# Performance work log

Hardware: AMD Instinct MI355X
Metric: run time of the kernel (lower is better)

Reference implementation:

```python
import jax, jax.numpy as jnp
import numpy as np

BS, HIST, H, W, NOBJ = 512, 3, 10, 10, 4
NSENT, TOK, DM = 3, 36, 768
EMB, FM, K, NL, ADIM = 256, 64, 2, 128, 5
LIN = FM * (H - (K - 1)) * (W - (K - 1))  # 64*9*9 = 5184
ATTN_SCALE = float(np.sqrt(EMB))  # 16.0


def setup_inputs() -> dict:
    key = jax.random.key(0)
    ks = jax.random.split(key, 24)
    g = lambda i, shape, s=0.02: jax.random.normal(ks[i], shape, dtype=jnp.float32) * s
    sprite_emb = g(0, (25, EMB), 1.0).at[0].set(0.0)  # padding_idx=0 -> zero row
    inp = {
        'state': jax.random.randint(ks[1], (BS, HIST, H, W, NOBJ), 0, 25, dtype=jnp.int32),
        'action': jax.random.randint(ks[2], (BS,), 0, ADIM, dtype=jnp.int32),
        'temb': jax.random.normal(ks[3], (BS, NSENT, TOK, DM), dtype=jnp.float32),
        'sprite_emb': sprite_emb,
        'conv_w': g(4, (K, K, HIST * EMB, FM)),  # HWIO
        'conv_b': g(5, (FM,)),
        'Wk': g(6, (DM, EMB)), 'bk': g(7, (EMB,)),
        'Wks': g(8, (DM, 1)), 'bks': g(9, (1,)),
        'Wv': g(10, (DM, EMB)), 'bv': g(11, (EMB,)),
        'Wvs': g(12, (DM, 1)), 'bvs': g(13, (1,)),
        'a1': g(14, (LIN, NL)), 'a1b': g(15, (NL,)),
        'a2': g(16, (NL, NL)), 'a2b': g(17, (NL,)),
        'a3': g(18, (NL, ADIM)), 'a3b': g(19, (ADIM,)),
        'v1': g(20, (LIN, NL)), 'v1b': g(21, (NL,)),
        'v2': g(22, (NL, NL)), 'v2b': g(23, (NL,)),
        'v3': jax.random.normal(jax.random.fold_in(key, 99), (NL, 1)) * 0.02,
        'v3b': jnp.zeros((1,), jnp.float32),
    }
    return inp


def _nonzero_mean(e):
    # e: [..., n, emb]; mean over rows that are nonzero (padding rows are all-zero)
    cnt = jnp.sum(jnp.sum(e, axis=-1) != 0, axis=-1, keepdims=True)
    return jnp.sum(e, axis=-2) / jnp.maximum(cnt, 1).astype(e.dtype)


def reference(state, action, temb, sprite_emb, conv_w, conv_b, Wk, bk, Wks, bks,
              Wv, bv, Wvs, bvs, a1, a1b, a2, a2b, a3, a3b, v1, v1b, v2, v2b, v3, v3b):
    lrelu = jax.nn.leaky_relu  # slope 0.01 matches torch default
    bs = state.shape[0]
    obj_state, avt_state = state[..., :-1], state[..., -1:]
    query = _nonzero_mean(sprite_emb[obj_state])   # [bs,hist,H,W,emb]
    avatar = _nonzero_mean(sprite_emb[avt_state])  # [bs,hist,H,W,emb]
    # text key/value: scaled token-softmax pooling over tokens (dim=2)
    k = (temb @ Wk + bk) * jax.nn.softmax(temb @ Wks + bks, axis=-2)
    k = jnp.sum(k, axis=2)                          # [bs,nsent,emb]
    v = (temb @ Wv + bv) * jax.nn.softmax(temb @ Wvs + bvs, axis=-2)
    v = jnp.sum(v, axis=2)                          # [bs,nsent,emb]
    # batch_attention
    q2 = query.reshape(bs, -1, EMB)                 # [bs, hist*H*W, emb]
    kq = jnp.einsum('bxe,bse->bxs', q2, k) / ATTN_SCALE
    wts = jax.nn.softmax(kq, axis=-1) * (kq != 0)
    wts = wts.reshape(bs, HIST, H, W, NSENT)
    # mean(weights[...,None]*value, dim=-2) == (w @ v) / nsent
    att = jnp.einsum('bthws,bse->bthwe', wts, v) / NSENT  # [bs,hist,H,W,emb]
    st = att.reshape(bs, H, W, -1)                  # fold hist into channels (768)
    av = avatar.reshape(bs, H, W, -1)
    st = (st + av) / 2.0                            # NHWC, C=768
    y = jax.lax.conv_general_dilated(st, conv_w, (1, 1), 'VALID',
                                     dimension_numbers=('NHWC', 'HWIO', 'NHWC')) + conv_b
    y = lrelu(y)                                    # [bs,9,9,64]
    y = jnp.transpose(y, (0, 3, 1, 2)).reshape(bs, -1)  # torch NCHW flatten order
    ha = lrelu(lrelu(y @ a1 + a1b) @ a2 + a2b)
    logits = ha @ a3 + a3b
    logp = jax.nn.log_softmax(logits, axis=-1)
    action_logprobs = jnp.take_along_axis(logp, action[:, None].astype(jnp.int32), axis=-1)[:, 0]
    entropy = -jnp.sum(jnp.exp(logp) * logp, axis=-1)
    hv = lrelu(lrelu(y @ v1 + v1b) @ v2 + v2b)
    state_value = (hv @ v3 + v3b)[:, 0]
    return action_logprobs, state_value, entropy
```

## Files before the change

### kernel.cpp

```cpp
#include <hip/hip_runtime.h>
#include <hip/hip_bf16.h>
#include <math.h>

constexpr int BS   = 512;
constexpr int NBS  = 1536;
constexpr int NPOS = 300;
constexpr int LIN  = 5184;
constexpr int KSPLIT = 9, KCH = 576;

typedef __attribute__((ext_vector_type(8))) short bf16x8;
typedef __attribute__((ext_vector_type(4))) float f32x4;

static __device__ __forceinline__ short f2bf(float f) {
    unsigned u = __float_as_uint(f);
    unsigned r = (u + 0x7FFFu + ((u >> 16) & 1u)) >> 16;
    return (short)r;
}
static __device__ __forceinline__ unsigned pk2(float a, float b) {
    return ((unsigned)(unsigned short)f2bf(a)) | (((unsigned)(unsigned short)f2bf(b)) << 16);
}
static __device__ __forceinline__ float bf2f_lo(unsigned u) { return __uint_as_float(u << 16); }
static __device__ __forceinline__ float bf2f_hi(unsigned u) { return __uint_as_float(u & 0xFFFF0000u); }

constexpr size_t OFF_RD   = 0;
constexpr size_t OFF_FL   = 19968;
constexpr size_t OFF_DT   = 20032;
constexpr size_t OFF_WCT  = 118336;
constexpr size_t OFF_PH   = 413248;
constexpr size_t OFF_AB   = 437824;
constexpr size_t OFF_XKH  = 1101376;
constexpr size_t OFF_XVH  = 1691200;
constexpr size_t OFF_VWH  = 2281024;
constexpr size_t OFF_YH   = 2870848;
constexpr size_t OFF_PART = 4197952;

__global__ __launch_bounds__(512) void k1_fused(
    const float* __restrict__ temb, const float* __restrict__ Wks,
    const float* __restrict__ Wvs, const float* __restrict__ conv_w,
    const float* __restrict__ sprite, const float* __restrict__ Wk,
    const float* __restrict__ Wv, const float* __restrict__ bv,
    const float* __restrict__ a1, const float* __restrict__ v1,
    short* __restrict__ XKH, short* __restrict__ XVH,
    short* __restrict__ AB, short* __restrict__ PH, short* __restrict__ WCT,
    float* __restrict__ RD, int* __restrict__ FL)
{
    __shared__ unsigned smem[13824 + 160];
    unsigned* hbuf = smem;
    float (*sco)[40] = (float(*)[40])(smem + 13824);
    int tid = threadIdx.x, bx = blockIdx.x;
    int lane = tid & 63, w = tid >> 6;

    if (bx < NBS) {
        int bs = bx;
        const float4* src4 = (const float4*)temb + (size_t)bs * 6912;

        #pragma unroll
        for (int c = 0; c < 7; ++c) {
            int i = c * 512 + tid;
            if (c < 6 || tid < 384) {
                float4 v = src4[i];
                hbuf[2 * i]     = pk2(v.x, v.y);
                hbuf[2 * i + 1] = pk2(v.z, v.w);
            }
        }
        __syncthreads();

        float4 q0, q1, q2, q3, q4, q5, q6 = make_float4(0.f, 0.f, 0.f, 0.f);
        q0 = src4[3456 + tid];
        q1 = src4[3968 + tid];
        q2 = src4[4480 + tid];
        q3 = src4[4992 + tid];
        q4 = src4[5504 + tid];
        q5 = src4[6016 + tid];
        if (tid < 384) q6 = src4[6528 + tid];

        const float2* wks2 = (const float2*)Wks;
        const float2* wvs2 = (const float2*)Wvs;
        #pragma unroll
        for (int rr = 0; rr < 3; ++rr) {
            int t = w + 8 * rr;
            if (rr < 2 || w < 2) {
                float pk = 0.f, pv = 0.f;
                #pragma unroll
                for (int j = 0; j < 6; ++j) {
                    unsigned u = hbuf[t * 384 + lane + 64 * j];
                    float x0 = bf2f_lo(u), x1 = bf2f_hi(u);
                    float2 a = wks2[lane + 64 * j];
                    float2 b = wvs2[lane + 64 * j];
                    pk += x0 * a.x + x1 * a.y;
                    pv += x0 * b.x + x1 * b.y;
                }
                #pragma unroll
                for (int off = 32; off; off >>= 1) {
                    pk += __shfl_down(pk, off);
                    pv += __shfl_down(pv, off);
                }
                if (lane == 0) { sco[0][t] = pk; sco[1][t] = pv; }
            }
        }

        hbuf[2 * (3456 + tid)]     = pk2(q0.x, q0.y);
        hbuf[2 * (3456 + tid) + 1] = pk2(q0.z, q0.w);
        hbuf[2 * (3968 + tid)]     = pk2(q1.x, q1.y);
        hbuf[2 * (3968 + tid) + 1] = pk2(q1.z, q1.w);
        hbuf[2 * (4480 + tid)]     = pk2(q2.x, q2.y);
        hbuf[2 * (4480 + tid) + 1] = pk2(q2.z, q2.w);
        hbuf[2 * (4992 + tid)]     = pk2(q3.x, q3.y);
        hbuf[2 * (4992 + tid) + 1] = pk2(q3.z, q3.w);
        hbuf[2 * (5504 + tid)]     = pk2(q4.x, q4.y);
        hbuf[2 * (5504 + tid) + 1] = pk2(q4.z, q4.w);
        hbuf[2 * (6016 + tid)]     = pk2(q5.x, q5.y);
        hbuf[2 * (6016 + tid) + 1] = pk2(q5.z, q5.w);
        if (tid < 384) {
            hbuf[2 * (6528 + tid)]     = pk2(q6.x, q6.y);
            hbuf[2 * (6528 + tid) + 1] = pk2(q6.z, q6.w);
        }
        __syncthreads();

        #pragma unroll
        for (int rr = 0; rr < 3; ++rr) {
            int t = 18 + w + 8 * rr;
            if (rr < 2 || w < 2) {
                float pk = 0.f, pv = 0.f;
                #pragma unroll
                for (int j = 0; j < 6; ++j) {
                    unsigned u = hbuf[t * 384 + lane + 64 * j];
                    float x0 = bf2f_lo(u), x1 = bf2f_hi(u);
                    float2 a = wks2[lane + 64 * j];
                    float2 b = wvs2[lane + 64 * j];
                    pk += x0 * a.x + x1 * a.y;
                    pv += x0 * b.x + x1 * b.y;
                }
                #pragma unroll
                for (int off = 32; off; off >>= 1) {
                    pk += __shfl_down(pk, off);
                    pv += __shfl_down(pv, off);
                }
                if (lane == 0) { sco[0][t] = pk; sco[1][t] = pv; }
            }
        }
        __syncthreads();

        if (w < 2) {
            float s = (lane < 36) ? sco[w][lane] : -INFINITY;
            float m = s;
            #pragma unroll
            for (int off = 32; off; off >>= 1) m = fmaxf(m, __shfl_xor(m, off));
            float e = (lane < 36) ? expf(s - m) : 0.f;
            float z = e;
            #pragma unroll
            for (int off = 32; off; off >>= 1) z += __shfl_xor(z, off);
            if (lane < 36) sco[2 + w][lane] = e / z;
        }
        __syncthreads();

        if (tid < 384) {
            float k0 = 0.f, k1 = 0.f, v0 = 0.f, v1 = 0.f;
            #pragma unroll
            for (int t = 0; t < 36; ++t) {
                unsigned u = hbuf[t * 384 + tid];
                float x0 = bf2f_lo(u), x1 = bf2f_hi(u);
                float wk = sco[2][t], wv = sco[3][t];
                k0 += wk * x0; k1 += wk * x1;
                v0 += wv * x0; v1 += wv * x1;
            }
            ((unsigned*)XKH)[(size_t)bs * 384 + tid] = pk2(k0, k1);
            ((unsigned*)XVH)[(size_t)bs * 384 + tid] = pk2(v0, v1);
        }
        return;
    }

    int id = bx - NBS;
    if (id < 324) {
        float (*tile)[65] = (float(*)[65])smem;
        int kt = id % 81, nt = id / 81;
        const float* src = (nt < 2) ? a1 : v1;
        int col0 = (nt & 1) * 64;
        #pragma unroll
        for (int it = 0; it < 8; ++it) {
            int idx = it * 512 + tid; int ki = idx >> 6, ni = idx & 63;
            tile[ki][ni] = src[(size_t)(kt * 64 + ki) * 128 + col0 + ni];
        }
        __syncthreads();
        #pragma unroll
        for (int it = 0; it < 8; ++it) {
            int idx = it * 512 + tid; int ni = idx >> 6, ki = idx & 63;
            AB[(size_t)(nt * 64 + ni) * 5184 + kt * 64 + ki] = f2bf(tile[ki][ni]);
        }
    } else if (id < 362) {
        int g = (id - 324) * 512 + tid;
        if (g < 19200) {
            int o = g / 768, d = g - o * 768;
            const float* sp = sprite + o * 256;
            const float* wr = Wk + (size_t)d * 256;
            float s = 0.f;
            for (int c = 0; c < 256; ++c) s += sp[c] * wr[c];
            PH[(size_t)o * 768 + d] = f2bf(s);
        }
    } else if (id < 401) {
        int g = (id - 362) * 512 + tid;
        if (g < 19968) {
            int o = g / 768, n = g - o * 768;
            int tap = n >> 6, f = n & 63; int t4 = tap / 3, j = tap - t4 * 3;
            const float* sp = (o < 25) ? (sprite + o * 256) : bv;
            float s = 0.f;
            for (int e = 0; e < 256; ++e)
                s += sp[e] * conv_w[(size_t)(t4 * 768 + j * 256 + e) * 64 + f];
            RD[g] = s;
        }
    } else if (id < 545) {
        int wid2 = id - 401;
        int bm = (wid2 / 12) * 64, bn = (wid2 % 12) * 64;
        int p = bm >> 6; int t4 = p / 3, jj = p - t4 * 3;
        const float* cwb = conv_w + (size_t)(t4 * 768 + jj * 256) * 64;
        float* As = (float*)smem;
        float* Bs = (float*)smem + 4160;
        float acc[4][4];
        #pragma unroll
        for (int i = 0; i < 4; ++i)
            #pragma unroll
            for (int j = 0; j < 4; ++j) acc[i][j] = 0.f;
        int tm = (tid & 255) >> 4, tn = tid & 15;
        for (int kc = 0; kc < 256; kc += 64) {
            #pragma unroll
            for (int it = 0; it < 8; ++it) {
                int idx = it * 512 + tid; int c = idx >> 6, f = idx & 63;
                As[c * 65 + f] = cwb[(size_t)(kc + c) * 64 + f];
            }
            #pragma unroll
            for (int it = 0; it < 8; ++it) {
                int idx = it * 512 + tid; int d = idx >> 6, c = idx & 63;
                Bs[c * 65 + d] = Wv[(size_t)(bn + d) * 256 + kc + c];
            }
            __syncthreads();
            if (tid < 256) {
                for (int kk = 0; kk < 64; ++kk) {
                    float a[4], b[4];
                    #pragma unroll
                    for (int i = 0; i < 4; ++i) a[i] = As[kk * 65 + tm * 4 + i];
                    #pragma unroll
                    for (int j = 0; j < 4; ++j) b[j] = Bs[kk * 65 + tn * 4 + j];
                    #pragma unroll
                    for (int i = 0; i < 4; ++i)
                        #pragma unroll
                        for (int j = 0; j < 4; ++j) acc[i][j] += a[i] * b[j];
                }
            }
            __syncthreads();
        }
        if (tid < 256) {
            #pragma unroll
            for (int i = 0; i < 4; ++i)
                #pragma unroll
                for (int j = 0; j < 4; ++j)
                    WCT[(size_t)(bm + tm * 4 + i) * 768 + bn + tn * 4 + j] = f2bf(acc[i][j]);
        }
    } else {
        if (tid < 25) {
            float s = 0.f;
            for (int c = 0; c < 256; ++c) s += sprite[tid * 256 + c];
            FL[tid] = (s != 0.0f) ? 1 : 0;
        }
    }
}

template<int BIAS, int OUTBF>
__global__ __launch_bounds__(256) void gemm_mfma(
    const short* __restrict__ A, const short* __restrict__ B,
    const float* __restrict__ bias, void* __restrict__ Cout,
    int K, int ldc, int klen, size_t czstride)
{
    __shared__ short As[64][40];
    __shared__ short Bs[64][40];
    int tid = threadIdx.x;
    int bm = blockIdx.x * 64, bn = blockIdx.y * 64;
    int wid = tid >> 6, lane = tid & 63;
    int wm = (wid >> 1) * 32, wn = (wid & 1) * 32;
    int l15 = lane & 15, lg = lane >> 4;

    f32x4 zero = {0.f, 0.f, 0.f, 0.f};
    f32x4 acc00 = zero, acc01 = zero, acc10 = zero, acc11 = zero;

    int srow = tid >> 2, kch = (tid & 3) * 8;
    const short* Ap = A + (size_t)(bm + srow) * K + kch + (size_t)blockIdx.z * klen;
    const short* Bp = B + (size_t)(bn + srow) * K + kch + (size_t)blockIdx.z * klen;

    for (int kt = 0; kt < klen; kt += 32) {
        bf16x8 aval = *(const bf16x8*)(Ap + kt);
        bf16x8 bval = *(const bf16x8*)(Bp + kt);
        *(bf16x8*)&As[srow][kch] = aval;
        *(bf16x8*)&Bs[srow][kch] = bval;
        __syncthreads();
        bf16x8 af0 = *(const bf16x8*)&As[wm + l15][lg * 8];
        bf16x8 af1 = *(const bf16x8*)&As[wm + 16 + l15][lg * 8];
        bf16x8 bg0 = *(const bf16x8*)&Bs[wn + l15][lg * 8];
        bf16x8 bg1 = *(const bf16x8*)&Bs[wn + 16 + l15][lg * 8];
        acc00 = __builtin_amdgcn_mfma_f32_16x16x32_bf16(af0, bg0, acc00, 0, 0, 0);
        acc01 = __builtin_amdgcn_mfma_f32_16x16x32_bf16(af0, bg1, acc01, 0, 0, 0);
        acc10 = __builtin_amdgcn_mfma_f32_16x16x32_bf16(af1, bg0, acc10, 0, 0, 0);
        acc11 = __builtin_amdgcn_mfma_f32_16x16x32_bf16(af1, bg1, acc11, 0, 0, 0);
        __syncthreads();
    }

    float* Cf = (float*)Cout + (size_t)blockIdx.z * czstride;
    short* Ch = (short*)Cout;
    #pragma unroll
    for (int i = 0; i < 2; ++i) {
        f32x4 arow0 = (i == 0) ? acc00 : acc10;
        f32x4 arow1 = (i == 0) ? acc01 : acc11;
        #pragma unroll
        for (int j = 0; j < 2; ++j) {
            f32x4 a = (j == 0) ? arow0 : arow1;
            int col = bn + wn + j * 16 + l15;
            float bb = BIAS ? bias[col] : 0.f;
            #pragma unroll
            for (int r = 0; r < 4; ++r) {
                int row = bm + wm + i * 16 + lg * 4 + r;
                float v = a[r] + bb;
                if (OUTBF) Ch[(size_t)row * ldc + col] = f2bf(v);
                else       Cf[(size_t)row * ldc + col] = v;
            }
        }
    }
}

__global__ __launch_bounds__(256) void k3_vwdt(
    const short* __restrict__ XVH, const short* __restrict__ WCT,
    const float* __restrict__ bvW2, short* __restrict__ VWH,
    const short* __restrict__ XKH, const short* __restrict__ PH,
    float* __restrict__ DT)
{
    __shared__ short As[64][40];
    __shared__ short Bs[64][40];
    int tid = threadIdx.x;
    bool isdt = (blockIdx.y == 12);
    const short* A = isdt ? XKH : XVH;
    const short* B = isdt ? PH  : WCT;
    int bm = blockIdx.x * 64, bn = isdt ? 0 : blockIdx.y * 64;
    int wid = tid >> 6, lane = tid & 63;
    int wm = (wid >> 1) * 32, wn = (wid & 1) * 32;
    int l15 = lane & 15, lg = lane >> 4;

    f32x4 zero = {0.f, 0.f, 0.f, 0.f};
    f32x4 acc00 = zero, acc01 = zero, acc10 = zero, acc11 = zero;

    int srow = tid >> 2, kch = (tid & 3) * 8;
    const short* Ap = A + (size_t)(bm + srow) * 768 + kch;
    const short* Bp = B + (size_t)(bn + srow) * 768 + kch;

    for (int kt = 0; kt < 768; kt += 32) {
        bf16x8 aval = *(const bf16x8*)(Ap + kt);
        bf16x8 bval = *(const bf16x8*)(Bp + kt);
        *(bf16x8*)&As[srow][kch] = aval;
        *(bf16x8*)&Bs[srow][kch] = bval;
        __syncthreads();
        bf16x8 af0 = *(const bf16x8*)&As[wm + l15][lg * 8];
        bf16x8 af1 = *(const bf16x8*)&As[wm + 16 + l15][lg * 8];
        bf16x8 bg0 = *(const bf16x8*)&Bs[wn + l15][lg * 8];
        bf16x8 bg1 = *(const bf16x8*)&Bs[wn + 16 + l15][lg * 8];
        acc00 = __builtin_amdgcn_mfma_f32_16x16x32_bf16(af0, bg0, acc00, 0, 0, 0);
        acc01 = __builtin_amdgcn_mfma_f32_16x16x32_bf16(af0, bg1, acc01, 0, 0, 0);
        acc10 = __builtin_amdgcn_mfma_f32_16x16x32_bf16(af1, bg0, acc10, 0, 0, 0);
        acc11 = __builtin_amdgcn_mfma_f32_16x16x32_bf16(af1, bg1, acc11, 0, 0, 0);
        __syncthreads();
    }

    #pragma unroll
    for (int i = 0; i < 2; ++i) {
        f32x4 arow0 = (i == 0) ? acc00 : acc10;
        f32x4 arow1 = (i == 0) ? acc01 : acc11;
        #pragma unroll
        for (int j = 0; j < 2; ++j) {
            f32x4 a = (j == 0) ? arow0 : arow1;
            int col = bn + wn + j * 16 + l15;
            #pragma unroll
            for (int r = 0; r < 4; ++r) {
                int row = bm + wm + i * 16 + lg * 4 + r;
                if (isdt) DT[(size_t)row * 64 + col] = a[r];
                else      VWH[(size_t)row * 768 + col] = f2bf(a[r] + bvW2[col]);
            }
        }
    }
}

__global__ __launch_bounds__(512) void k4_y(
    const int* __restrict__ state, const float* __restrict__ dt,
    const int* __restrict__ flags, const short* __restrict__ VWH,
    const float* __restrict__ rowdot, const float* __restrict__ conv_b,
    short* __restrict__ y)
{
    int b = blockIdx.x, tid = threadIdx.x;
    __shared__ float s_vW[3 * 768];
    __shared__ float s_w[3][NPOS + 4];
    __shared__ int   s_avt[NPOS + 4];
    __shared__ float s_y[81 * 65];

    const unsigned* vr = (const unsigned*)(VWH + (size_t)b * 3 * 768);
    for (int i = tid; i < 1152; i += 512) {
        unsigned u = vr[i];
        s_vW[2 * i]     = bf2f_lo(u);
        s_vW[2 * i + 1] = bf2f_hi(u);
    }

    for (int code = tid; code < NPOS; code += 512) {
        const int* st = state + ((size_t)b * NPOS + code) * 4;
        int o0 = st[0], o1 = st[1], o2 = st[2], avi = st[3];
        int cnt = flags[o0] + flags[o1] + flags[o2];
        s_avt[code] = avi;
        float w0 = 0.f, w1 = 0.f, w2 = 0.f;
        if (cnt > 0) {
            const float* d0 = dt + (size_t)b * 192;
            float inv = 1.0f / (16.0f * (float)cnt);
            float q0 = (d0[o0]       + d0[o1]       + d0[o2])       * inv;
            float q1 = (d0[64 + o0]  + d0[64 + o1]  + d0[64 + o2])  * inv;
            float q2 = (d0[128 + o0] + d0[128 + o1] + d0[128 + o2]) * inv;
            float m = fmaxf(q0, fmaxf(q1, q2));
            float e0 = expf(q0 - m), e1 = expf(q1 - m), e2 = expf(q2 - m);
            float is = 1.0f / (6.0f * (e0 + e1 + e2));
            w0 = e0 * is; w1 = e1 * is; w2 = e2 * is;
        }
        s_w[0][code] = w0; s_w[1][code] = w1; s_w[2][code] = w2;
    }
    __syncthreads();

    int f = tid & 63;
    float cb = conv_b[f];
    for (int p = tid >> 6; p < 81; p += 8) {
        int oh = p / 9, ow = p - oh * 9;
        float acc = cb;
        #pragma unroll
        for (int kh = 0; kh < 2; ++kh)
        #pragma unroll
        for (int kw = 0; kw < 2; ++kw) {
            int bc = 3 * ((oh + kh) * 10 + (ow + kw));
            int tbase = ((kh * 2 + kw) * 3) * 64 + f;
            #pragma unroll
            for (int j = 0; j < 3; ++j) {
                int code = bc + j;
                int tf = tbase + j * 64;
                acc += s_w[0][code] * s_vW[tf]
                     + s_w[1][code] * s_vW[768 + tf]
                     + s_w[2][code] * s_vW[2 * 768 + tf];
                acc += 0.5f * rowdot[(size_t)s_avt[code] * 768 + tf];
            }
        }
        acc = acc > 0.f ? acc : 0.01f * acc;
        s_y[p * 65 + f] = acc;
    }
    __syncthreads();
    for (int i = tid; i < LIN; i += 512) {
        int ff = i / 81, pp = i - ff * 81;
        y[(size_t)b * LIN + i] = f2bf(s_y[pp * 65 + ff]);
    }
}

__global__ __launch_bounds__(128) void k6_heads(
    const float* __restrict__ PART, const float* __restrict__ a1b,
    const float* __restrict__ v1b, const int* __restrict__ action,
    const float* __restrict__ a2, const float* __restrict__ a2b,
    const float* __restrict__ a3, const float* __restrict__ a3b,
    const float* __restrict__ v2, const float* __restrict__ v2b,
    const float* __restrict__ v3, const float* __restrict__ v3b,
    float* __restrict__ out)
{
    int b = blockIdx.x, tid = threadIdx.x;
    __shared__ float h1a[128], h1v[128], h2a[128], red[128];
    __shared__ float lg[5];
    float sa0 = a1b[tid], sv0 = v1b[tid];
    const float* pb = PART + (size_t)b * 256;
    for (int z = 0; z < KSPLIT; ++z) {
        sa0 += pb[(size_t)z * (BS * 256) + tid];
        sv0 += pb[(size_t)z * (BS * 256) + 128 + tid];
    }
    h1a[tid] = sa0 > 0.f ? sa0 : 0.01f * sa0;
    h1v[tid] = sv0 > 0.f ? sv0 : 0.01f * sv0;
    __syncthreads();
    float sa = a2b[tid], sv = v2b[tid];
    for (int k = 0; k < 128; ++k) {
        sa += h1a[k] * a2[k * 128 + tid];
        sv += h1v[k] * v2[k * 128 + tid];
    }
    sa = sa > 0.f ? sa : 0.01f * sa;
    sv = sv > 0.f ? sv : 0.01f * sv;
    h2a[tid] = sa;
    red[tid] = sv * v3[tid];
    __syncthreads();
    for (int s = 64; s > 0; s >>= 1) {
        if (tid < s) red[tid] += red[tid + s];
        __syncthreads();
    }
    if (tid < 5) {
        float l = a3b[tid];
        for (int k = 0; k < 128; ++k) l += h2a[k] * a3[k * 5 + tid];
        lg[tid] = l;
    }
    __syncthreads();
    if (tid == 0) {
        float m = lg[0];
        for (int j2 = 1; j2 < 5; ++j2) m = fmaxf(m, lg[j2]);
        float se = 0.f;
        for (int j2 = 0; j2 < 5; ++j2) se += expf(lg[j2] - m);
        float lse = m + logf(se);
        int act = action[b];
        float ent = 0.f;
        for (int j2 = 0; j2 < 5; ++j2) {
            float lp = lg[j2] - lse;
            ent -= expf(lp) * lp;
        }
        out[b]        = lg[act] - lse;
        out[512 + b]  = red[0] + v3b[0];
        out[1024 + b] = ent;
    }
}

extern "C" void kernel_launch(void* const* d_in, const int* in_sizes, int n_in,
                              void* d_out, int out_size, void* d_ws, size_t ws_size,
                              hipStream_t stream)
{
    const int*   state  = (const int*)d_in[0];
    const int*   action = (const int*)d_in[1];
    const float* temb   = (const float*)d_in[2];
    const float* sprite = (const float*)d_in[3];
    const float* conv_w = (const float*)d_in[4];
    const float* conv_b = (const float*)d_in[5];
    const float* Wk     = (const float*)d_in[6];
    const float* Wks    = (const float*)d_in[8];
    const float* Wv     = (const float*)d_in[10];
    const float* bv     = (const float*)d_in[11];
    const float* Wvs    = (const float*)d_in[12];
    const float* a1     = (const float*)d_in[14];
    const float* a1b    = (const float*)d_in[15];
    const float* a2     = (const float*)d_in[16];
    const float* a2b    = (const float*)d_in[17];
    const float* a3     = (const float*)d_in[18];
    const float* a3b    = (const float*)d_in[19];
    const float* v1     = (const float*)d_in[20];
    const float* v1b    = (const float*)d_in[21];
    const float* v2     = (const float*)d_in[22];
    const float* v2b    = (const float*)d_in[23];
    const float* v3     = (const float*)d_in[24];
    const float* v3b    = (const float*)d_in[25];
    (void)in_sizes; (void)n_in; (void)out_size; (void)ws_size;

    float* ws  = (float*)d_ws;
    float* RD  = ws + OFF_RD;
    float* bvW2= RD + 25 * 768;
    int*   FL  = (int*)(ws + OFF_FL);
    float* DT  = ws + OFF_DT;
    short* WCT = (short*)(ws + OFF_WCT);
    short* PH  = (short*)(ws + OFF_PH);
    short* AB  = (short*)(ws + OFF_AB);
    short* XKH = (short*)(ws + OFF_XKH);
    short* XVH = (short*)(ws + OFF_XVH);
    short* VWH = (short*)(ws + OFF_VWH);
    short* YH  = (short*)(ws + OFF_YH);
    float* PART= ws + OFF_PART;
    float* out = (float*)d_out;

    k1_fused<<<NBS + 546, 512, 0, stream>>>(
        temb, Wks, Wvs, conv_w, sprite, Wk, Wv, bv, a1, v1,
        XKH, XVH, AB, PH, WCT, RD, FL);
    k3_vwdt<<<dim3(24,13,1),256,0,stream>>>(XVH, WCT, bvW2, VWH, XKH, PH, DT);
    k4_y<<<BS, 512, 0, stream>>>(state, DT, FL, VWH, RD, conv_b, YH);
    gemm_mfma<0,0><<<dim3(8,4,KSPLIT),256,0,stream>>>(YH, AB, nullptr, PART, 5184, 256, KCH, (size_t)BS*256);
    k6_heads<<<BS, 128, 0, stream>>>(PART, a1b, v1b, action, a2, a2b, a3, a3b,
                                     v2, v2b, v3, v3b, out);
}
```

Measured before the change: 128.7 us.

## Load text embeddings in one pass and shrink k1 shared memory

The text-pooling block now converts the first 34 tokens of each sentence to bf16 in shared memory in a single pass. The earlier version did two phases with register staging and an extra barrier. The last two tokens are never staged: their score dot products and weighted sums read fp32 directly from global memory. This cuts the shared-memory footprint, and the conv/Wv weight-combine tile drops from a 64 to a 32 k-chunk, also to lower LDS use and raise occupancy. It also rearranges buffer offsets and moves the gemm_mfma definition, at the cost of some repeated global reads for the tail tokens.

```diff
diff --git a/kernel.cpp b/kernel.cpp
--- a/kernel.cpp
+++ b/kernel.cpp
@@ -21,6 +21,8 @@
 }
 static __device__ __forceinline__ float bf2f_lo(unsigned u) { return __uint_as_float(u << 16); }
 static __device__ __forceinline__ float bf2f_hi(unsigned u) { return __uint_as_float(u & 0xFFFF0000u); }
+
+#define DOT4(a,b) ((a).x*(b).x + (a).y*(b).y + (a).z*(b).z + (a).w*(b).w)
 
 constexpr size_t OFF_RD   = 0;
 constexpr size_t OFF_FL   = 19968;
@@ -28,11 +30,11 @@
 constexpr size_t OFF_WCT  = 118336;
 constexpr size_t OFF_PH   = 413248;
 constexpr size_t OFF_AB   = 437824;
-constexpr size_t OFF_XKH  = 1101376;
-constexpr size_t OFF_XVH  = 1691200;
-constexpr size_t OFF_VWH  = 2281024;
-constexpr size_t OFF_YH   = 2870848;
-constexpr size_t OFF_PART = 4197952;
+constexpr size_t OFF_XKH  = 1322560;
+constexpr size_t OFF_XVH  = 1912384;
+constexpr size_t OFF_VWH  = 2502208;
+constexpr size_t OFF_YH   = 3092032;
+constexpr size_t OFF_PART = 4419136;
 
 __global__ __launch_bounds__(512) void k1_fused(
     const float* __restrict__ temb, const float* __restrict__ Wks,
@@ -44,100 +46,85 @@
     short* __restrict__ AB, short* __restrict__ PH, short* __restrict__ WCT,
     float* __restrict__ RD, int* __restrict__ FL)
 {
-    __shared__ unsigned smem[13824 + 160];
+    __shared__ unsigned smem[13056 + 160];
     unsigned* hbuf = smem;
-    float (*sco)[40] = (float(*)[40])(smem + 13824);
+    float (*sco)[40] = (float(*)[40])(smem + 13056);
     int tid = threadIdx.x, bx = blockIdx.x;
-    int lane = tid & 63, w = tid >> 6;
+    int w = tid >> 6, lane = tid & 63;
 
     if (bx < NBS) {
         int bs = bx;
-        const float4* src4 = (const float4*)temb + (size_t)bs * 6912;
-
-        #pragma unroll
-        for (int c = 0; c < 7; ++c) {
+        const f32x4* src4 = (const f32x4*)temb + (size_t)bs * 6912;
+
+        #pragma unroll
+        for (int c = 0; c < 13; ++c) {
             int i = c * 512 + tid;
-            if (c < 6 || tid < 384) {
-                float4 v = src4[i];
+            if (c < 12 || i < 6528) {
+                f32x4 v = src4[i];
                 hbuf[2 * i]     = pk2(v.x, v.y);
                 hbuf[2 * i + 1] = pk2(v.z, v.w);
             }
         }
         __syncthreads();
 
-        float4 q0, q1, q2, q3, q4, q5, q6 = make_float4(0.f, 0.f, 0.f, 0.f);
-        q0 = src4[3456 + tid];
-        q1 = src4[3968 + tid];
-        q2 = src4[4480 + tid];
-        q3 = src4[4992 + tid];
-        q4 = src4[5504 + tid];
-        q5 = src4[6016 + tid];
-        if (tid < 384) q6 = src4[6528 + tid];
-
         const float2* wks2 = (const float2*)Wks;
         const float2* wvs2 = (const float2*)Wvs;
         #pragma unroll
-        for (int rr = 0; rr < 3; ++rr) {
-            int t = w + 8 * rr;
-            if (rr < 2 || w < 2) {
-                float pk = 0.f, pv = 0.f;
-                #pragma unroll
-                for (int j = 0; j < 6; ++j) {
-                    unsigned u = hbuf[t * 384 + lane + 64 * j];
-                    float x0 = bf2f_lo(u), x1 = bf2f_hi(u);
-                    float2 a = wks2[lane + 64 * j];
-                    float2 b = wvs2[lane + 64 * j];
-                    pk += x0 * a.x + x1 * a.y;
-                    pv += x0 * b.x + x1 * b.y;
-                }
-                #pragma unroll
-                for (int off = 32; off; off >>= 1) {
-                    pk += __shfl_down(pk, off);
-                    pv += __shfl_down(pv, off);
-                }
-                if (lane == 0) { sco[0][t] = pk; sco[1][t] = pv; }
-            }
-        }
-
-        hbuf[2 * (3456 + tid)]     = pk2(q0.x, q0.y);
-        hbuf[2 * (3456 + tid) + 1] = pk2(q0.z, q0.w);
-        hbuf[2 * (3968 + tid)]     = pk2(q1.x, q1.y);
-        hbuf[2 * (3968 + tid) + 1] = pk2(q1.z, q1.w);
-        hbuf[2 * (4480 + tid)]     = pk2(q2.x, q2.y);
-        hbuf[2 * (4480 + tid) + 1] = pk2(q2.z, q2.w);
-        hbuf[2 * (4992 + tid)]     = pk2(q3.x, q3.y);
-        hbuf[2 * (4992 + tid) + 1] = pk2(q3.z, q3.w);
-        hbuf[2 * (5504 + tid)]     = pk2(q4.x, q4.y);
-        hbuf[2 * (5504 + tid) + 1] = pk2(q4.z, q4.w);
-        hbuf[2 * (6016 + tid)]     = pk2(q5.x, q5.y);
-        hbuf[2 * (6016 + tid) + 1] = pk2(q5.z, q5.w);
-        if (tid < 384) {
-            hbuf[2 * (6528 + tid)]     = pk2(q6.x, q6.y);
-            hbuf[2 * (6528 + tid) + 1] = pk2(q6.z, q6.w);
-        }
-        __syncthreads();
-
-        #pragma unroll
-        for (int rr = 0; rr < 3; ++rr) {
-            int t = 18 + w + 8 * rr;
-            if (rr < 2 || w < 2) {
-                float pk = 0.f, pv = 0.f;
-                #pragma unroll
-                for (int j = 0; j < 6; ++j) {
-                    unsigned u = hbuf[t * 384 + lane + 64 * j];
-                    float x0 = bf2f_lo(u), x1 = bf2f_hi(u);
-                    float2 a = wks2[lane + 64 * j];
-                    float2 b = wvs2[lane + 64 * j];
-                    pk += x0 * a.x + x1 * a.y;
-                    pv += x0 * b.x + x1 * b.y;
-                }
-                #pragma unroll
-                for (int off = 32; off; off >>= 1) {
-                    pk += __shfl_down(pk, off);
-                    pv += __shfl_down(pv, off);
-                }
-                if (lane == 0) { sco[0][t] = pk; sco[1][t] = pv; }
-            }
+        for (int r = 0; r < 4; ++r) {
+            int t = w + 8 * r;
+            float pk = 0.f, pv = 0.f;
+            #pragma unroll
+            for (int j = 0; j < 6; ++j) {
+                unsigned u = hbuf[t * 384 + lane + 64 * j];
+                float x0 = bf2f_lo(u), x1 = bf2f_hi(u);
+                float2 a = wks2[lane + 64 * j];
+                float2 b = wvs2[lane + 64 * j];
+                pk += x0 * a.x + x1 * a.y;
+                pv += x0 * b.x + x1 * b.y;
+            }
+            #pragma unroll
+            for (int off = 32; off; off >>= 1) {
+                pk += __shfl_down(pk, off);
+                pv += __shfl_down(pv, off);
+            }
+            if (lane == 0) { sco[0][t] = pk; sco[1][t] = pv; }
+        }
+        if (w < 2) {
+            int t = 32 + w;
+            float pk = 0.f, pv = 0.f;
+            #pragma unroll
+            for (int j = 0; j < 6; ++j) {
+                unsigned u = hbuf[t * 384 + lane + 64 * j];
+                float x0 = bf2f_lo(u), x1 = bf2f_hi(u);
+                float2 a = wks2[lane + 64 * j];
+                float2 b = wvs2[lane + 64 * j];
+                pk += x0 * a.x + x1 * a.y;
+                pv += x0 * b.x + x1 * b.y;
+            }
+            #pragma unroll
+            for (int off = 32; off; off >>= 1) {
+                pk += __shfl_down(pk, off);
+                pv += __shfl_down(pv, off);
+            }
+            if (lane == 0) { sco[0][t] = pk; sco[1][t] = pv; }
+        } else if (w < 4) {
+            int t = 32 + w;
+            const f32x4* row = src4 + (size_t)t * 192;
+            const f32x4* k4 = (const f32x4*)Wks;
+            const f32x4* v4 = (const f32x4*)Wvs;
+            float pk = 0.f, pv = 0.f;
+            #pragma unroll
+            for (int i = 0; i < 3; ++i) {
+                f32x4 x = row[lane + 64 * i];
+                pk += DOT4(x, k4[lane + 64 * i]);
+                pv += DOT4(x, v4[lane + 64 * i]);
+            }
+            #pragma unroll
+            for (int off = 32; off; off >>= 1) {
+                pk += __shfl_down(pk, off);
+                pv += __shfl_down(pv, off);
+            }
+            if (lane == 0) { sco[0][t] = pk; sco[1][t] = pv; }
         }
         __syncthreads();
 
@@ -157,13 +144,20 @@
         if (tid < 384) {
             float k0 = 0.f, k1 = 0.f, v0 = 0.f, v1 = 0.f;
             #pragma unroll
-            for (int t = 0; t < 36; ++t) {
+            for (int t = 0; t < 34; ++t) {
                 unsigned u = hbuf[t * 384 + tid];
                 float x0 = bf2f_lo(u), x1 = bf2f_hi(u);
                 float wk = sco[2][t], wv = sco[3][t];
                 k0 += wk * x0; k1 += wk * x1;
                 v0 += wv * x0; v1 += wv * x1;
             }
+            const float* rowb = temb + (size_t)bs * 27648;
+            float2 g34 = *(const float2*)(rowb + 34 * 768 + 2 * tid);
+            float2 g35 = *(const float2*)(rowb + 35 * 768 + 2 * tid);
+            k0 += sco[2][34] * g34.x + sco[2][35] * g35.x;
+            k1 += sco[2][34] * g34.y + sco[2][35] * g35.y;
+            v0 += sco[3][34] * g34.x + sco[3][35] * g35.x;
+            v1 += sco[3][34] * g34.y + sco[3][35] * g35.y;
             ((unsigned*)XKH)[(size_t)bs * 384 + tid] = pk2(k0, k1);
             ((unsigned*)XVH)[(size_t)bs * 384 + tid] = pk2(v0, v1);
         }
@@ -214,27 +208,25 @@
         int p = bm >> 6; int t4 = p / 3, jj = p - t4 * 3;
         const float* cwb = conv_w + (size_t)(t4 * 768 + jj * 256) * 64;
         float* As = (float*)smem;
-        float* Bs = (float*)smem + 4160;
+        float* Bs = (float*)smem + 2080;
         float acc[4][4];
         #pragma unroll
         for (int i = 0; i < 4; ++i)
             #pragma unroll
             for (int j = 0; j < 4; ++j) acc[i][j] = 0.f;
         int tm = (tid & 255) >> 4, tn = tid & 15;
-        for (int kc = 0; kc < 256; kc += 64) {
-            #pragma unroll
-            for (int it = 0; it < 8; ++it) {
-                int idx = it * 512 + tid; int c = idx >> 6, f = idx & 63;
-                As[c * 65 + f] = cwb[(size_t)(kc + c) * 64 + f];
-            }
-            #pragma unroll
-            for (int it = 0; it < 8; ++it) {
-                int idx = it * 512 + tid; int d = idx >> 6, c = idx & 63;
-                Bs[c * 65 + d] = Wv[(size_t)(bn + d) * 256 + kc + c];
+        for (int kc = 0; kc < 256; kc += 32) {
+            for (int idx = tid; idx < 2048; idx += 512) {
+                int cc = idx >> 6, f = idx & 63;
+                As[cc * 65 + f] = cwb[(size_t)(kc + cc) * 64 + f];
+            }
+            for (int idx = tid; idx < 2048; idx += 512) {
+                int d = idx >> 5, cc = idx & 31;
+                Bs[cc * 65 + d] = Wv[(size_t)(bn + d) * 256 + kc + cc];
             }
             __syncthreads();
             if (tid < 256) {
-                for (int kk = 0; kk < 64; ++kk) {
+                for (int kk = 0; kk < 32; ++kk) {
                     float a[4], b[4];
                     #pragma unroll
                     for (int i = 0; i < 4; ++i) a[i] = As[kk * 65 + tm * 4 + i];
@@ -260,66 +252,6 @@
             float s = 0.f;
             for (int c = 0; c < 256; ++c) s += sprite[tid * 256 + c];
             FL[tid] = (s != 0.0f) ? 1 : 0;
-        }
-    }
-}
-
-template<int BIAS, int OUTBF>
-__global__ __launch_bounds__(256) void gemm_mfma(
-    const short* __restrict__ A, const short* __restrict__ B,
-    const float* __restrict__ bias, void* __restrict__ Cout,
-    int K, int ldc, int klen, size_t czstride)
-{
-    __shared__ short As[64][40];
-    __shared__ short Bs[64][40];
-    int tid = threadIdx.x;
-    int bm = blockIdx.x * 64, bn = blockIdx.y * 64;
-    int wid = tid >> 6, lane = tid & 63;
-    int wm = (wid >> 1) * 32, wn = (wid & 1) * 32;
-    int l15 = lane & 15, lg = lane >> 4;
-
-    f32x4 zero = {0.f, 0.f, 0.f, 0.f};
-    f32x4 acc00 = zero, acc01 = zero, acc10 = zero, acc11 = zero;
-
-    int srow = tid >> 2, kch = (tid & 3) * 8;
-    const short* Ap = A + (size_t)(bm + srow) * K + kch + (size_t)blockIdx.z * klen;
-    const short* Bp = B + (size_t)(bn + srow) * K + kch + (size_t)blockIdx.z * klen;
-
-    for (int kt = 0; kt < klen; kt += 32) {
-        bf16x8 aval = *(const bf16x8*)(Ap + kt);
-        bf16x8 bval = *(const bf16x8*)(Bp + kt);
-        *(bf16x8*)&As[srow][kch] = aval;
-        *(bf16x8*)&Bs[srow][kch] = bval;
-        __syncthreads();
-        bf16x8 af0 = *(const bf16x8*)&As[wm + l15][lg * 8];
-        bf16x8 af1 = *(const bf16x8*)&As[wm + 16 + l15][lg * 8];
-        bf16x8 bg0 = *(const bf16x8*)&Bs[wn + l15][lg * 8];
-        bf16x8 bg1 = *(const bf16x8*)&Bs[wn + 16 + l15][lg * 8];
-        acc00 = __builtin_amdgcn_mfma_f32_16x16x32_bf16(af0, bg0, acc00, 0, 0, 0);
-        acc01 = __builtin_amdgcn_mfma_f32_16x16x32_bf16(af0, bg1, acc01, 0, 0, 0);
-        acc10 = __builtin_amdgcn_mfma_f32_16x16x32_bf16(af1, bg0, acc10, 0, 0, 0);
-        acc11 = __builtin_amdgcn_mfma_f32_16x16x32_bf16(af1, bg1, acc11, 0, 0, 0);
-        __syncthreads();
-    }
-
-    float* Cf = (float*)Cout + (size_t)blockIdx.z * czstride;
-    short* Ch = (short*)Cout;
-    #pragma unroll
-    for (int i = 0; i < 2; ++i) {
-        f32x4 arow0 = (i == 0) ? acc00 : acc10;
-        f32x4 arow1 = (i == 0) ? acc01 : acc11;
-        #pragma unroll
-        for (int j = 0; j < 2; ++j) {
-            f32x4 a = (j == 0) ? arow0 : arow1;
-            int col = bn + wn + j * 16 + l15;
-            float bb = BIAS ? bias[col] : 0.f;
-            #pragma unroll
-            for (int r = 0; r < 4; ++r) {
-                int row = bm + wm + i * 16 + lg * 4 + r;
-                float v = a[r] + bb;
-                if (OUTBF) Ch[(size_t)row * ldc + col] = f2bf(v);
-                else       Cf[(size_t)row * ldc + col] = v;
-            }
         }
     }
 }
@@ -378,6 +310,66 @@
                 int row = bm + wm + i * 16 + lg * 4 + r;
                 if (isdt) DT[(size_t)row * 64 + col] = a[r];
                 else      VWH[(size_t)row * 768 + col] = f2bf(a[r] + bvW2[col]);
+            }
+        }
+    }
+}
+
+template<int BIAS, int OUTBF>
+__global__ __launch_bounds__(256) void gemm_mfma(
+    const short* __restrict__ A, const short* __restrict__ B,
+    const float* __restrict__ bias, void* __restrict__ Cout,
+    int K, int ldc, int klen, size_t czstride)
+{
+    __shared__ short As[64][40];
+    __shared__ short Bs[64][40];
+    int tid = threadIdx.x;
+    int bm = blockIdx.x * 64, bn = blockIdx.y * 64;
+    int wid = tid >> 6, lane = tid & 63;
+    int wm = (wid >> 1) * 32, wn = (wid & 1) * 32;
+    int l15 = lane & 15, lg = lane >> 4;
+
+    f32x4 zero = {0.f, 0.f, 0.f, 0.f};
+    f32x4 acc00 = zero, acc01 = zero, acc10 = zero, acc11 = zero;
+
+    int srow = tid >> 2, kch = (tid & 3) * 8;
+    const short* Ap = A + (size_t)(bm + srow) * K + kch + (size_t)blockIdx.z * klen;
+    const short* Bp = B + (size_t)(bn + srow) * K + kch + (size_t)blockIdx.z * klen;
+
+    for (int kt = 0; kt < klen; kt += 32) {
+        bf16x8 aval = *(const bf16x8*)(Ap + kt);
+        bf16x8 bval = *(const bf16x8*)(Bp + kt);
+        *(bf16x8*)&As[srow][kch] = aval;
+        *(bf16x8*)&Bs[srow][kch] = bval;
+        __syncthreads();
+        bf16x8 af0 = *(const bf16x8*)&As[wm + l15][lg * 8];
+        bf16x8 af1 = *(const bf16x8*)&As[wm + 16 + l15][lg * 8];
+        bf16x8 bg0 = *(const bf16x8*)&Bs[wn + l15][lg * 8];
+        bf16x8 bg1 = *(const bf16x8*)&Bs[wn + 16 + l15][lg * 8];
+        acc00 = __builtin_amdgcn_mfma_f32_16x16x32_bf16(af0, bg0, acc00, 0, 0, 0);
+        acc01 = __builtin_amdgcn_mfma_f32_16x16x32_bf16(af0, bg1, acc01, 0, 0, 0);
+        acc10 = __builtin_amdgcn_mfma_f32_16x16x32_bf16(af1, bg0, acc10, 0, 0, 0);
+        acc11 = __builtin_amdgcn_mfma_f32_16x16x32_bf16(af1, bg1, acc11, 0, 0, 0);
+        __syncthreads();
+    }
+
+    float* Cf = (float*)Cout + (size_t)blockIdx.z * czstride;
+    short* Ch = (short*)Cout;
+    #pragma unroll
+    for (int i = 0; i < 2; ++i) {
+        f32x4 arow0 = (i == 0) ? acc00 : acc10;
+        f32x4 arow1 = (i == 0) ? acc01 : acc11;
+        #pragma unroll
+        for (int j = 0; j < 2; ++j) {
+            f32x4 a = (j == 0) ? arow0 : arow1;
+            int col = bn + wn + j * 16 + l15;
+            float bb = BIAS ? bias[col] : 0.f;
+            #pragma unroll
+            for (int r = 0; r < 4; ++r) {
+                int row = bm + wm + i * 16 + lg * 4 + r;
+                float v = a[r] + bb;
+                if (OUTBF) Ch[(size_t)row * ldc + col] = f2bf(v);
+                else       Cf[(size_t)row * ldc + col] = v;
             }
         }
     }
```

After: 123.4 us (median of 2 runs). -4.1%, faster.
